# Kernel optimization log

Measured on AMD Instinct MI355X. Metric: run time of the kernel, lower is better.

Reference implementation:

```python
import jax, jax.numpy as jnp
import numpy as np

HIDDEN = 4096
NUM_HEADS = 32
NUM_KV_HEADS = 8
HEAD_DIM = 128
T = 2048
ROPE_THETA = 10000.0


def setup_inputs() -> dict:
    key = jax.random.key(0)
    ks = jax.random.split(key, 10)
    s = 0.02
    return {
        "hidden_states": jax.random.normal(ks[0], (T, HIDDEN), dtype=jnp.float32),
        "positions": jnp.arange(T, dtype=jnp.int32),
        "Wq": jax.random.normal(ks[1], (NUM_HEADS * HEAD_DIM, HIDDEN), dtype=jnp.float32) * s,
        "bq": jax.random.normal(ks[2], (NUM_HEADS * HEAD_DIM,), dtype=jnp.float32) * s,
        "Wk": jax.random.normal(ks[3], (NUM_KV_HEADS * HEAD_DIM, HIDDEN), dtype=jnp.float32) * s,
        "bk": jax.random.normal(ks[4], (NUM_KV_HEADS * HEAD_DIM,), dtype=jnp.float32) * s,
        "Wv": jax.random.normal(ks[5], (NUM_KV_HEADS * HEAD_DIM, HIDDEN), dtype=jnp.float32) * s,
        "bv": jax.random.normal(ks[6], (NUM_KV_HEADS * HEAD_DIM,), dtype=jnp.float32) * s,
        "Wo": jax.random.normal(ks[7], (HIDDEN, HIDDEN), dtype=jnp.float32) * s,
        "bo": jax.random.normal(ks[8], (HIDDEN,), dtype=jnp.float32) * s,
    }


def _rope_cos_sin(positions, head_dim, base):
    # neox-style rotary over the full head_dim
    half = head_dim // 2
    inv_freq = 1.0 / (base ** (jnp.arange(0, half, dtype=jnp.float32) * 2.0 / head_dim))
    angles = positions.astype(jnp.float32)[:, None] * inv_freq[None, :]  # [T, half]
    return jnp.cos(angles), jnp.sin(angles)


def _apply_rope(x, cos, sin):
    # x: [T, H, D]; neox: split halves, rotate
    half = x.shape[-1] // 2
    x1, x2 = x[..., :half], x[..., half:]
    c = cos[:, None, :]
    s = sin[:, None, :]
    return jnp.concatenate([x1 * c - x2 * s, x2 * c + x1 * s], axis=-1)


def reference(hidden_states, positions, Wq, bq, Wk, bk, Wv, bv, Wo, bo):
    q = (hidden_states @ Wq.T + bq).reshape(T, NUM_HEADS, HEAD_DIM)
    k = (hidden_states @ Wk.T + bk).reshape(T, NUM_KV_HEADS, HEAD_DIM)
    v = (hidden_states @ Wv.T + bv).reshape(T, NUM_KV_HEADS, HEAD_DIM)

    cos, sin = _rope_cos_sin(positions, HEAD_DIM, ROPE_THETA)
    q = _apply_rope(q, cos, sin)
    k = _apply_rope(k, cos, sin)

    scale = 1.0 / np.sqrt(HEAD_DIM).astype(np.float32)
    group = NUM_HEADS // NUM_KV_HEADS
    qg = q.reshape(T, NUM_KV_HEADS, group, HEAD_DIM)
    # scores: [g_kv, r, q, k] without materializing repeated KV heads
    scores = jnp.einsum('qgrd,kgd->grqk', qg, k) * scale
    causal = positions[:, None] >= positions[None, :]  # [T, T]
    scores = jnp.where(causal[None, None], scores, jnp.finfo(scores.dtype).min)
    probs = jax.nn.softmax(scores, axis=-1)
    o = jnp.einsum('grqk,kgd->qgrd', probs, v).reshape(T, NUM_HEADS * HEAD_DIM)
    return o @ Wo.T + bo
```

## Files before the change

### kernel.cpp

```cpp
#include <hip/hip_runtime.h>
#include <stdint.h>

typedef unsigned short u16;
typedef __bf16 bf16x8_t __attribute__((ext_vector_type(8)));
typedef float f32x4_t __attribute__((ext_vector_type(4)));

#define T_SEQ 2048
#define HID 4096
#define ROWQKV 6144

__device__ __forceinline__ float bf2f(u16 x){ return __uint_as_float(((uint32_t)x)<<16); }
__device__ __forceinline__ u16 f2bf(float f){
  uint32_t u = __float_as_uint(f);
  return (u16)((u + 0x7fffu + ((u>>16)&1u)) >> 16);
}

__device__ __forceinline__ void gload16(const void* g, void* l){
  __builtin_amdgcn_global_load_lds(
      (const __attribute__((address_space(1))) uint32_t*)g,
      (__attribute__((address_space(3))) uint32_t*)l, 16, 0, 0);
}

__device__ __forceinline__ uint32_t cvtpk(float lo, float hi_){
  uint32_t r;
  asm("v_cvt_pk_bf16_f32 %0, %1, %2" : "=v"(r) : "v"(lo), "v"(hi_));
  return r;
}

__global__ void cvt_kernel(const float* __restrict__ src, u16* __restrict__ dst, int n8){
  int i = blockIdx.x*blockDim.x + threadIdx.x;
  if (i >= n8) return;
  const float4* s = (const float4*)src;
  float4 a = s[2*i], b = s[2*i+1];
  union { u16 u[8]; uint4 v; } o;
  o.u[0]=f2bf(a.x); o.u[1]=f2bf(a.y); o.u[2]=f2bf(a.z); o.u[3]=f2bf(a.w);
  o.u[4]=f2bf(b.x); o.u[5]=f2bf(b.y); o.u[6]=f2bf(b.z); o.u[7]=f2bf(b.w);
  ((uint4*)dst)[i] = o.v;
}

__global__ void setup_kernel(const float* __restrict__ bq, const float* __restrict__ bk,
                             const float* __restrict__ bv, const int* __restrict__ pos,
                             float* __restrict__ bqkv, float* __restrict__ cost,
                             float* __restrict__ sint){
  int i = blockIdx.x*blockDim.x + threadIdx.x;
  if (i < 6144) bqkv[i] = (i<4096) ? bq[i] : ((i<5120) ? bk[i-4096] : bv[i-5120]);
  if (i < T_SEQ*64){
    int t = i >> 6, d = i & 63;
    float inv = powf(10000.0f, -(float)(2*d) / 128.0f);
    float ang = (float)pos[t] * inv;
    cost[i] = cosf(ang);
    sint[i] = sinf(ang);
  }
}

#define GBAR __builtin_amdgcn_s_barrier()
#define LGKM0 do{ asm volatile("s_waitcnt lgkmcnt(0)" ::: "memory"); \
                  __builtin_amdgcn_sched_barrier(0); }while(0)

#define BUF6 28672

#define AREAD6(mh, ck) do{ \
  const u16* ab = &lds[cur + aoff + (mh)*4096]; \
  afr[0] = *(const bf16x8_t*)&ab[0*1024 + (ck)]; \
  afr[1] = *(const bf16x8_t*)&ab[1*1024 + (ck)]; \
  afr[2] = *(const bf16x8_t*)&ab[2*1024 + (ck)]; \
  afr[3] = *(const bf16x8_t*)&ab[3*1024 + (ck)]; }while(0)

#define BREAD6(ck) do{ \
  const u16* bb = &lds[cur + boff]; \
  bfr[0] = *(const bf16x8_t*)&bb[0*1024 + (ck)]; \
  bfr[1] = *(const bf16x8_t*)&bb[1*1024 + (ck)]; \
  bfr[2] = *(const bf16x8_t*)&bb[2*1024 + (ck)]; }while(0)

#define MM12(mh) do{ \
  _Pragma("unroll") \
  for (int mi=0; mi<4; ++mi){ \
    _Pragma("unroll") \
    for (int n=0; n<3; ++n) \
      acc[(mh)*4+mi][n] = __builtin_amdgcn_mfma_f32_16x16x32_bf16(afr[mi], bfr[n], acc[(mh)*4+mi][n],0,0,0); \
  } }while(0)

__global__ __launch_bounds__(512, 2)
void gemm_qkv(const u16* __restrict__ A, const u16* __restrict__ B,
              const float* __restrict__ bias, u16* __restrict__ Cb,
              int K, int N)
{
  __shared__ u16 lds[2*BUF6];
  const int tid = threadIdx.x, lane = tid & 63, w = tid >> 6;
  const int l15 = lane & 15, l4 = lane >> 4;
  const int wm = w >> 2, wn = w & 3;

  const int nwg = gridDim.x * gridDim.y;
  int flat = blockIdx.y * gridDim.x + blockIdx.x;
  flat = (flat & 7) * (nwg >> 3) + (flat >> 3);
  const int bx = flat % gridDim.x, by = flat / gridDim.x;
  const int bm = by * 256, bn = bx * 192;

  const int srow = w*8 + (lane >> 3);
  const int swc  = ((lane & 7) ^ (lane >> 3)) * 8;
  const u16* pA = A + (size_t)(bm + srow)*K + swc;
  const u16* pB = B + (size_t)(bn + srow)*K + swc;
  const size_t j64 = (size_t)64*K;
  const int wu = w*512;

  const int cA0 = ((0 + l4) ^ (l15 & 7)) * 8;
  const int cA1 = ((4 + l4) ^ (l15 & 7)) * 8;
  const int aoff = (wm*128 + l15) * 64;
  const int boff = 16384 + (wn*48 + l15) * 64;

  f32x4_t acc[8][3] = {};
  const int KT = K >> 6;

  gload16(pA + 0*j64, &lds[0     + wu]);
  gload16(pA + 1*j64, &lds[4096  + wu]);
  gload16(pA + 2*j64, &lds[8192  + wu]);
  gload16(pA + 3*j64, &lds[12288 + wu]);
  gload16(pB + 0*j64, &lds[16384 + wu]);
  gload16(pB + 1*j64, &lds[20480 + wu]);
  gload16(pB + 2*j64, &lds[24576 + wu]);
  pA += 64; pB += 64;
  asm volatile("s_waitcnt vmcnt(0)" ::: "memory");
  GBAR;

  for (int t = 0; t < KT; ++t){
    const int cur = (t & 1) * BUF6;
    const int nxt = ((t + 1) & 1) * BUF6;
    const bool st = (t + 1 < KT);
    bf16x8_t afr[4], bfr[3];

    BREAD6(cA0); AREAD6(0, cA0);
    if (st){
      gload16(pA + 0*j64, &lds[nxt + 0     + wu]);
      gload16(pA + 1*j64, &lds[nxt + 4096  + wu]);
      gload16(pA + 2*j64, &lds[nxt + 8192  + wu]);
      gload16(pA + 3*j64, &lds[nxt + 12288 + wu]);
    }
    GBAR; LGKM0;
    __builtin_amdgcn_s_setprio(1); MM12(0); __builtin_amdgcn_s_setprio(0);
    GBAR;

    AREAD6(1, cA0);
    if (st){
      gload16(pB + 0*j64, &lds[nxt + 16384 + wu]);
      gload16(pB + 1*j64, &lds[nxt + 20480 + wu]);
      gload16(pB + 2*j64, &lds[nxt + 24576 + wu]);
      pA += 64; pB += 64;
    }
    GBAR; LGKM0;
    __builtin_amdgcn_s_setprio(1); MM12(1); __builtin_amdgcn_s_setprio(0);
    GBAR;

    BREAD6(cA1); AREAD6(0, cA1);
    GBAR; LGKM0;
    __builtin_amdgcn_s_setprio(1); MM12(0); __builtin_amdgcn_s_setprio(0);
    GBAR;

    AREAD6(1, cA1);
    GBAR; LGKM0;
    __builtin_amdgcn_s_setprio(1); MM12(1); __builtin_amdgcn_s_setprio(0);
    if (st) asm volatile("s_waitcnt vmcnt(0)" ::: "memory");
    GBAR;
  }

  #pragma unroll
  for (int m=0;m<8;m++){
    #pragma unroll
    for (int n=0;n<3;n++){
      #pragma unroll
      for (int j=0;j<4;j++){
        int row = bm + wm*128 + (m>>2)*64 + (m&3)*16 + l4*4 + j;
        int col = bn + wn*48 + n*16 + l15;
        Cb[(size_t)row*N + col] = f2bf(acc[m][n][j] + bias[col]);
      }
    }
  }
}

#define BUFK 24576

#define KMREAD(ck) do{ \
  afr[0] = *(const bf16x8_t*)&lds[cur + aoff + 0*1024 + (ck)]; \
  afr[1] = *(const bf16x8_t*)&lds[cur + aoff + 1*1024 + (ck)]; \
  afr[2] = *(const bf16x8_t*)&lds[cur + aoff + 2*1024 + (ck)]; \
  afr[3] = *(const bf16x8_t*)&lds[cur + aoff + 3*1024 + (ck)]; \
  bfr[0] = *(const bf16x8_t*)&lds[cur + boff + 0*1024 + (ck)]; \
  bfr[1] = *(const bf16x8_t*)&lds[cur + boff + 1*1024 + (ck)]; \
  bfr[2] = *(const bf16x8_t*)&lds[cur + boff + 2*1024 + (ck)]; \
  bfr[3] = *(const bf16x8_t*)&lds[cur + boff + 3*1024 + (ck)]; }while(0)

#define MM16KM do{ \
  _Pragma("unroll") \
  for (int mi=0; mi<4; ++mi){ \
    _Pragma("unroll") \
    for (int n=0; n<4; ++n) \
      acc[mi][n] = __builtin_amdgcn_mfma_f32_16x16x32_bf16(afr[mi], bfr[n], acc[mi][n],0,0,0); \
  } }while(0)

__global__ __launch_bounds__(512, 2)
void gemm_km(const u16* __restrict__ A, const u16* __restrict__ B,
             const float* __restrict__ bias, float* __restrict__ Cf,
             int K, int N)
{
  __shared__ u16 lds[3*BUFK];
  const int tid = threadIdx.x, lane = tid & 63, w = tid >> 6;
  const int l15 = lane & 15, l4 = lane >> 4;
  const int wm = w >> 1, wn = w & 1;

  const int nwg = gridDim.x * gridDim.y;
  int flat = blockIdx.y * gridDim.x + blockIdx.x;
  flat = (flat & 7) * (nwg >> 3) + (flat >> 3);
  const int bx = flat % gridDim.x, by = flat / gridDim.x;
  const int bm = by * 256, bn = bx * 128;

  const int srow = w*8 + (lane >> 3);
  const int swc  = ((lane & 7) ^ (lane >> 3)) * 8;
  const u16* pA = A + (size_t)(bm + srow)*K + swc;
  const u16* pB = B + (size_t)(bn + srow)*K + swc;
  const size_t j64 = (size_t)64*K;
  const int wu = w*512;

  const int cA0 = ((0 + l4) ^ (l15 & 7)) * 8;
  const int cA1 = ((4 + l4) ^ (l15 & 7)) * 8;
  const int aoff = (wm*64 + l15) * 64;
  const int boff = 16384 + (wn*64 + l15) * 64;

  f32x4_t acc[4][4] = {};
  const int KT = K >> 6;

  gload16(pA + 0*j64,      &lds[0*4096 + wu]);
  gload16(pA + 1*j64,      &lds[1*4096 + wu]);
  gload16(pA + 2*j64,      &lds[2*4096 + wu]);
  gload16(pA + 3*j64,      &lds[3*4096 + wu]);
  gload16(pB + 0*j64,      &lds[16384 + 0*4096 + wu]);
  gload16(pB + 1*j64,      &lds[16384 + 1*4096 + wu]);
  gload16(pA + 64 + 0*j64, &lds[BUFK + 0*4096 + wu]);
  gload16(pA + 64 + 1*j64, &lds[BUFK + 1*4096 + wu]);
  gload16(pA + 64 + 2*j64, &lds[BUFK + 2*4096 + wu]);
  gload16(pA + 64 + 3*j64, &lds[BUFK + 3*4096 + wu]);
  gload16(pB + 64 + 0*j64, &lds[BUFK + 16384 + 0*4096 + wu]);
  gload16(pB + 64 + 1*j64, &lds[BUFK + 16384 + 1*4096 + wu]);
  pA += 128; pB += 128;
  asm volatile("s_waitcnt vmcnt(6)" ::: "memory");
  GBAR;

  for (int t = 0; t < KT; ++t){
    const int cur = (t % 3) * BUFK;
    const int sb  = ((t + 2) % 3) * BUFK;
    const bool st = (t + 2 < KT);
    bf16x8_t afr[4], bfr[4];

    KMREAD(cA0);
    if (st){
      gload16(pA + 0*j64, &lds[sb + 0*4096 + wu]);
      gload16(pA + 1*j64, &lds[sb + 1*4096 + wu]);
      gload16(pA + 2*j64, &lds[sb + 2*4096 + wu]);
    }
    GBAR; LGKM0;
    __builtin_amdgcn_s_setprio(1); MM16KM; __builtin_amdgcn_s_setprio(0);
    GBAR;

    KMREAD(cA1);
    if (st){
      gload16(pA + 3*j64, &lds[sb + 3*4096 + wu]);
      gload16(pB + 0*j64, &lds[sb + 16384 + 0*4096 + wu]);
      gload16(pB + 1*j64, &lds[sb + 16384 + 1*4096 + wu]);
      pA += 64; pB += 64;
    }
    GBAR; LGKM0;
    __builtin_amdgcn_s_setprio(1); MM16KM; __builtin_amdgcn_s_setprio(0);
    if (st)              asm volatile("s_waitcnt vmcnt(6)" ::: "memory");
    else if (t + 1 < KT) asm volatile("s_waitcnt vmcnt(0)" ::: "memory");
    GBAR;
  }

  #pragma unroll
  for (int mi=0;mi<4;mi++){
    #pragma unroll
    for (int n=0;n<4;n++){
      #pragma unroll
      for (int j=0;j<4;j++){
        int row = bm + wm*64 + mi*16 + l4*4 + j;
        int col = bn + wn*64 + n*16 + l15;
        Cf[(size_t)row*N + col] = acc[mi][n][j] + bias[col];
      }
    }
  }
}

__global__ void rope_kernel(u16* __restrict__ qkv, const float* __restrict__ cost,
                            const float* __restrict__ sint){
  int i = blockIdx.x*blockDim.x + threadIdx.x;
  int t = i / 2560;
  int r = i % 2560;
  int h = r >> 6, d = r & 63;
  int base = (h < 32) ? h*128 : (4096 + (h-32)*128);
  size_t p1 = (size_t)t*ROWQKV + base + d;
  float x1 = bf2f(qkv[p1]), x2 = bf2f(qkv[p1+64]);
  float c = cost[(t<<6)+d], s = sint[(t<<6)+d];
  qkv[p1]    = f2bf(x1*c - x2*s);
  qkv[p1+64] = f2bf(x2*c + x1*s);
}

#define VOFF 16384
#define POFF 24576

__global__ __launch_bounds__(256, 2)
void attn_kernel(const u16* __restrict__ qkv, u16* __restrict__ attn_o)
{
  __shared__ u16 lds[28672];
  const int tid = threadIdx.x, lane = tid&63, wid = tid>>6;
  const int l15 = lane&15, l4 = lane>>4;
  const int l7 = l15 & 7;
  const int h  = blockIdx.x & 31;
  const int qt = 31 - (blockIdx.x >> 5);
  const int q0 = qt * 64;
  const int kvh = h >> 2;
  const u16* Qg = qkv + h*128;
  const u16* Kg = qkv + 4096 + kvh*128;
  const u16* Vg = qkv + 5120 + kvh*128;
  const float c2 = 0.127543147f;

  bf16x8_t qf[4];
  {
    size_t qrow = (size_t)(q0 + wid*16 + l15);
    #pragma unroll
    for (int kk=0;kk<4;kk++)
      qf[kk] = *(const bf16x8_t*)(Qg + qrow*ROWQKV + kk*32 + l4*8);
  }
  float mrow[4] = {-1e30f,-1e30f,-1e30f,-1e30f};
  float lrow[4] = {0.f,0.f,0.f,0.f};
  f32x4_t oacc[8] = {};

  const u16* ksrc[4];
  int kls[4];
  #pragma unroll
  for (int i=0;i<4;i++){
    const int c = wid*4 + i;
    ksrc[i] = Kg + (size_t)((c&7)*8 + (lane>>3))*ROWQKV
               + (c>>3)*64 + ((lane&7)^(lane>>3))*8;
    kls[i] = c*512;
  }
  const int kvp = tid & 31;
  const int vd0 = (tid >> 5) * 16;
  uint4 rv[4];

  #pragma unroll
  for (int i=0;i<4;i++) gload16(ksrc[i], &lds[kls[i]]);
  #pragma unroll
  for (int i=0;i<4;i++) ksrc[i] += (size_t)64*ROWQKV;
  {
    const u16* va = Vg + (size_t)(2*kvp)*ROWQKV + vd0;
    rv[0] = *(const uint4*)va;            rv[1] = *(const uint4*)(va + 8);
    rv[2] = *(const uint4*)(va + ROWQKV); rv[3] = *(const uint4*)(va + ROWQKV + 8);
  }
  __syncthreads();
  {
    const u16* ra = (const u16*)&rv[0]; const u16* rb = (const u16*)&rv[2];
    #pragma unroll
    for (int e=0;e<8;e++)
      *(uint32_t*)&lds[VOFF + (vd0+e)*64 + ((kvp>>2)^(e&7))*8 + 2*(kvp&3)]
          = (uint32_t)ra[e] | ((uint32_t)rb[e] << 16);
    ra = (const u16*)&rv[1]; rb = (const u16*)&rv[3];
    #pragma unroll
    for (int e=0;e<8;e++)
      *(uint32_t*)&lds[VOFF + (vd0+8+e)*64 + ((kvp>>2)^(e&7))*8 + 2*(kvp&3)]
          = (uint32_t)ra[e] | ((uint32_t)rb[e] << 16);
  }
  __syncthreads();

  for (int kt = 0; kt <= qt; ++kt){
    const int kv0 = kt * 64;
    const int kcur = (kt & 1) * 8192;
    const bool pre = (kt < qt);
    if (pre){
      const int knxt = ((kt+1) & 1) * 8192;
      #pragma unroll
      for (int i=0;i<4;i++) gload16(ksrc[i], &lds[knxt + kls[i]]);
      #pragma unroll
      for (int i=0;i<4;i++) ksrc[i] += (size_t)64*ROWQKV;
      const u16* va = Vg + (size_t)(kv0 + 64 + 2*kvp)*ROWQKV + vd0;
      rv[0] = *(const uint4*)va;            rv[1] = *(const uint4*)(va + 8);
      rv[2] = *(const uint4*)(va + ROWQKV); rv[3] = *(const uint4*)(va + ROWQKV + 8);
    }

    f32x4_t sacc[4] = {};
    __builtin_amdgcn_s_setprio(1);
    #pragma unroll
    for (int n=0;n<4;n++){
      #pragma unroll
      for (int kk=0;kk<4;kk++){
        bf16x8_t kf = *(const bf16x8_t*)&lds[kcur + (kk>>1)*4096
                        + (n*16+l15)*64 + (((kk&1)*4 + l4) ^ l7)*8];
        sacc[n] = __builtin_amdgcn_mfma_f32_16x16x32_bf16(qf[kk], kf, sacc[n], 0,0,0);
      }
    }
    __builtin_amdgcn_s_setprio(0);
    float sv[4][4];
    float pmax[4] = {-1e30f,-1e30f,-1e30f,-1e30f};
    bool diag = (kt == qt);
    #pragma unroll
    for (int n=0;n<4;n++){
      int kvcol = kv0 + n*16 + l15;
      #pragma unroll
      for (int j=0;j<4;j++){
        float s = sacc[n][j];
        int qrow = q0 + wid*16 + l4*4 + j;
        if (diag && kvcol > qrow) s = -1e30f;
        sv[n][j] = s;
        pmax[j] = fmaxf(pmax[j], s);
      }
    }
    #pragma unroll
    for (int off=1; off<16; off<<=1){
      #pragma unroll
      for (int j=0;j<4;j++)
        pmax[j] = fmaxf(pmax[j], __shfl_xor(pmax[j], off, 64));
    }
    float esc[4], rsum[4] = {0.f,0.f,0.f,0.f}, mc[4];
    #pragma unroll
    for (int j=0;j<4;j++){
      float mn = fmaxf(mrow[j], pmax[j]);
      esc[j] = exp2f((mrow[j] - mn) * c2);
      mrow[j] = mn;
      mc[j] = mn * c2;
    }
    #pragma unroll
    for (int n=0;n<4;n++){
      #pragma unroll
      for (int j=0;j<4;j++){
        float p = exp2f(fmaf(sv[n][j], c2, -mc[j]));
        sv[n][j] = p;
        rsum[j] += p;
      }
    }
    #pragma unroll
    for (int off=1; off<16; off<<=1){
      #pragma unroll
      for (int j=0;j<4;j++)
        rsum[j] += __shfl_xor(rsum[j], off, 64);
    }
    #pragma unroll
    for (int j=0;j<4;j++) lrow[j] = lrow[j]*esc[j] + rsum[j];
    #pragma unroll
    for (int n=0;n<8;n++){
      #pragma unroll
      for (int j=0;j<4;j++) oacc[n][j] *= esc[j];
    }
    {
      const int r0 = wid*16 + l4*4;
      #pragma unroll
      for (int n=0;n<4;n++){
        uint32_t p01 = cvtpk(sv[n][0], sv[n][1]);
        uint32_t p23 = cvtpk(sv[n][2], sv[n][3]);
        const int cb = n*2 + (l15>>3);
        lds[POFF + (r0+0)*64 + ((cb ^ ((r0+0)&7))*8) + l7] = (u16)p01;
        lds[POFF + (r0+1)*64 + ((cb ^ ((r0+1)&7))*8) + l7] = (u16)(p01 >> 16);
        lds[POFF + (r0+2)*64 + ((cb ^ ((r0+2)&7))*8) + l7] = (u16)p23;
        lds[POFF + (r0+3)*64 + ((cb ^ ((r0+3)&7))*8) + l7] = (u16)(p23 >> 16);
      }
    }
    __builtin_amdgcn_s_setprio(1);
    #pragma unroll
    for (int kk=0;kk<2;kk++){
      const int blk = ((kk*4 + l4) ^ l7)*8;
      bf16x8_t pf = *(const bf16x8_t*)&lds[POFF + (wid*16 + l15)*64 + blk];
      #pragma unroll
      for (int n=0;n<8;n++){
        bf16x8_t vf = *(const bf16x8_t*)&lds[VOFF + (n*16 + l15)*64 + blk];
        oacc[n] = __builtin_amdgcn_mfma_f32_16x16x32_bf16(pf, vf, oacc[n], 0,0,0);
      }
    }
    __builtin_amdgcn_s_setprio(0);
    __syncthreads();
    if (pre){
      const u16* ra = (const u16*)&rv[0]; const u16* rb = (const u16*)&rv[2];
      #pragma unroll
      for (int e=0;e<8;e++)
        *(uint32_t*)&lds[VOFF + (vd0+e)*64 + ((kvp>>2)^(e&7))*8 + 2*(kvp&3)]
            = (uint32_t)ra[e] | ((uint32_t)rb[e] << 16);
      ra = (const u16*)&rv[1]; rb = (const u16*)&rv[3];
      #pragma unroll
      for (int e=0;e<8;e++)
        *(uint32_t*)&lds[VOFF + (vd0+8+e)*64 + ((kvp>>2)^(e&7))*8 + 2*(kvp&3)]
            = (uint32_t)ra[e] | ((uint32_t)rb[e] << 16);
    }
    __syncthreads();
  }

  #pragma unroll
  for (int n=0;n<8;n++){
    #pragma unroll
    for (int j=0;j<4;j++){
      int qrow = q0 + wid*16 + l4*4 + j;
      int col  = h*128 + n*16 + l15;
      attn_o[(size_t)qrow*HID + col] = f2bf(oacc[n][j] / lrow[j]);
    }
  }
}

extern "C" void kernel_launch(void* const* d_in, const int* in_sizes, int n_in,
                              void* d_out, int out_size, void* d_ws, size_t ws_size,
                              hipStream_t stream)
{
  const float* hs = (const float*)d_in[0];
  const int*  pos = (const int*)d_in[1];
  const float* Wq = (const float*)d_in[2];
  const float* bq = (const float*)d_in[3];
  const float* Wk = (const float*)d_in[4];
  const float* bk = (const float*)d_in[5];
  const float* Wv = (const float*)d_in[6];
  const float* bv = (const float*)d_in[7];
  const float* Wo = (const float*)d_in[8];
  const float* bo = (const float*)d_in[9];
  float* out = (float*)d_out;

  char* ws = (char*)d_ws;
  u16* hs_bf   = (u16*)ws;  ws += (size_t)2048*4096*2;
  u16* Wqkv_bf = (u16*)ws;  ws += (size_t)6144*4096*2;
  u16* Wo_bf   = (u16*)ws;  ws += (size_t)4096*4096*2;
  u16* qkv     = (u16*)ws;  ws += (size_t)2048*6144*2;
  u16* attn_b  = (u16*)ws;  ws += (size_t)2048*4096*2;
  float* bqkv  = (float*)ws; ws += (size_t)6144*4;
  float* cost  = (float*)ws; ws += (size_t)2048*64*4;
  float* sint  = (float*)ws; ws += (size_t)2048*64*4;

  {
    int n8 = 2048*4096/8;
    cvt_kernel<<<(n8+255)/256, 256, 0, stream>>>(hs, hs_bf, n8);
    n8 = 4096*4096/8;
    cvt_kernel<<<(n8+255)/256, 256, 0, stream>>>(Wq, Wqkv_bf, n8);
    n8 = 1024*4096/8;
    cvt_kernel<<<(n8+255)/256, 256, 0, stream>>>(Wk, Wqkv_bf + (size_t)4096*4096, n8);
    cvt_kernel<<<(n8+255)/256, 256, 0, stream>>>(Wv, Wqkv_bf + (size_t)5120*4096, n8);
    n8 = 4096*4096/8;
    cvt_kernel<<<(n8+255)/256, 256, 0, stream>>>(Wo, Wo_bf, n8);
  }
  setup_kernel<<<(T_SEQ*64 + 255)/256, 256, 0, stream>>>(bq, bk, bv, pos, bqkv, cost, sint);

  gemm_qkv<<<dim3(6144/192, 2048/256), 512, 0, stream>>>(hs_bf, Wqkv_bf, bqkv, qkv, 4096, 6144);
  rope_kernel<<<(T_SEQ*40*64)/256, 256, 0, stream>>>(qkv, cost, sint);
  attn_kernel<<<1024, 256, 0, stream>>>(qkv, attn_b);
  gemm_km<<<dim3(4096/128, 2048/256), 512, 0, stream>>>(attn_b, Wo_bf, bo, out, 4096, 4096);
}
```

Baseline: 341.2 us.

## Use 128-row query tiles with 8 waves and double-buffered V in attention

```diff
diff --git a/kernel.cpp b/kernel.cpp
--- a/kernel.cpp
+++ b/kernel.cpp
@@ -302,27 +302,30 @@
 }
 
 #define VOFF 16384
-#define POFF 24576
-
-__global__ __launch_bounds__(256, 2)
+#define POFF 32768
+
+__global__ __launch_bounds__(512, 4)
 void attn_kernel(const u16* __restrict__ qkv, u16* __restrict__ attn_o)
 {
-  __shared__ u16 lds[28672];
+  __shared__ u16 lds[40960];
   const int tid = threadIdx.x, lane = tid&63, wid = tid>>6;
   const int l15 = lane&15, l4 = lane>>4;
   const int l7 = l15 & 7;
-  const int h  = blockIdx.x & 31;
-  const int qt = 31 - (blockIdx.x >> 5);
-  const int q0 = qt * 64;
+  const int b = blockIdx.x;
+  const int h = b & 31;
+  const int c = (b < 256) ? (15 - (b >> 5)) : ((b - 256) >> 5);
+  const int qb = c * 128;
+  const int qwb = qb + wid*16;
   const int kvh = h >> 2;
   const u16* Qg = qkv + h*128;
   const u16* Kg = qkv + 4096 + kvh*128;
   const u16* Vg = qkv + 5120 + kvh*128;
   const float c2 = 0.127543147f;
+  const int nt = 2*c + 2;
 
   bf16x8_t qf[4];
   {
-    size_t qrow = (size_t)(q0 + wid*16 + l15);
+    size_t qrow = (size_t)(qwb + l15);
     #pragma unroll
     for (int kk=0;kk<4;kk++)
       qf[kk] = *(const bf16x8_t*)(Qg + qrow*ROWQKV + kk*32 + l4*8);
@@ -331,157 +334,146 @@
   float lrow[4] = {0.f,0.f,0.f,0.f};
   f32x4_t oacc[8] = {};
 
-  const u16* ksrc[4];
-  int kls[4];
+  const u16* ksrc[2];
+  int kls[2];
   #pragma unroll
-  for (int i=0;i<4;i++){
-    const int c = wid*4 + i;
-    ksrc[i] = Kg + (size_t)((c&7)*8 + (lane>>3))*ROWQKV
-               + (c>>3)*64 + ((lane&7)^(lane>>3))*8;
-    kls[i] = c*512;
+  for (int i=0;i<2;i++){
+    const int cc = wid*2 + i;
+    ksrc[i] = Kg + (size_t)((cc&7)*8 + (lane>>3))*ROWQKV
+               + (cc>>3)*64 + ((lane&7)^(lane>>3))*8;
+    kls[i] = cc*512;
   }
   const int kvp = tid & 31;
-  const int vd0 = (tid >> 5) * 16;
-  uint4 rv[4];
-
-  #pragma unroll
-  for (int i=0;i<4;i++) gload16(ksrc[i], &lds[kls[i]]);
-  #pragma unroll
-  for (int i=0;i<4;i++) ksrc[i] += (size_t)64*ROWQKV;
+  const int vd0 = (tid >> 5) * 8;
+  uint4 rv[2];
+
+  gload16(ksrc[0], &lds[kls[0]]);
+  gload16(ksrc[1], &lds[kls[1]]);
+  ksrc[0] += (size_t)64*ROWQKV; ksrc[1] += (size_t)64*ROWQKV;
   {
     const u16* va = Vg + (size_t)(2*kvp)*ROWQKV + vd0;
-    rv[0] = *(const uint4*)va;            rv[1] = *(const uint4*)(va + 8);
-    rv[2] = *(const uint4*)(va + ROWQKV); rv[3] = *(const uint4*)(va + ROWQKV + 8);
-  }
-  __syncthreads();
-  {
-    const u16* ra = (const u16*)&rv[0]; const u16* rb = (const u16*)&rv[2];
+    rv[0] = *(const uint4*)va;
+    rv[1] = *(const uint4*)(va + ROWQKV);
+    const u16* ra = (const u16*)&rv[0]; const u16* rb = (const u16*)&rv[1];
     #pragma unroll
     for (int e=0;e<8;e++)
-      *(uint32_t*)&lds[VOFF + (vd0+e)*64 + ((kvp>>2)^(e&7))*8 + 2*(kvp&3)]
+      *(uint32_t*)&lds[VOFF + (vd0+e)*64 + ((kvp>>2)^e)*8 + 2*(kvp&3)]
           = (uint32_t)ra[e] | ((uint32_t)rb[e] << 16);
-    ra = (const u16*)&rv[1]; rb = (const u16*)&rv[3];
-    #pragma unroll
-    for (int e=0;e<8;e++)
-      *(uint32_t*)&lds[VOFF + (vd0+8+e)*64 + ((kvp>>2)^(e&7))*8 + 2*(kvp&3)]
-          = (uint32_t)ra[e] | ((uint32_t)rb[e] << 16);
   }
   __syncthreads();
 
-  for (int kt = 0; kt <= qt; ++kt){
+  for (int kt = 0; kt < nt; ++kt){
     const int kv0 = kt * 64;
     const int kcur = (kt & 1) * 8192;
-    const bool pre = (kt < qt);
+    const int vcur = VOFF + (kt & 1) * 8192;
+    const bool pre = (kt + 1 < nt);
     if (pre){
       const int knxt = ((kt+1) & 1) * 8192;
-      #pragma unroll
-      for (int i=0;i<4;i++) gload16(ksrc[i], &lds[knxt + kls[i]]);
-      #pragma unroll
-      for (int i=0;i<4;i++) ksrc[i] += (size_t)64*ROWQKV;
+      gload16(ksrc[0], &lds[knxt + kls[0]]);
+      gload16(ksrc[1], &lds[knxt + kls[1]]);
+      ksrc[0] += (size_t)64*ROWQKV; ksrc[1] += (size_t)64*ROWQKV;
       const u16* va = Vg + (size_t)(kv0 + 64 + 2*kvp)*ROWQKV + vd0;
-      rv[0] = *(const uint4*)va;            rv[1] = *(const uint4*)(va + 8);
-      rv[2] = *(const uint4*)(va + ROWQKV); rv[3] = *(const uint4*)(va + ROWQKV + 8);
-    }
-
-    f32x4_t sacc[4] = {};
-    __builtin_amdgcn_s_setprio(1);
-    #pragma unroll
-    for (int n=0;n<4;n++){
-      #pragma unroll
-      for (int kk=0;kk<4;kk++){
-        bf16x8_t kf = *(const bf16x8_t*)&lds[kcur + (kk>>1)*4096
-                        + (n*16+l15)*64 + (((kk&1)*4 + l4) ^ l7)*8];
-        sacc[n] = __builtin_amdgcn_mfma_f32_16x16x32_bf16(qf[kk], kf, sacc[n], 0,0,0);
-      }
-    }
-    __builtin_amdgcn_s_setprio(0);
-    float sv[4][4];
-    float pmax[4] = {-1e30f,-1e30f,-1e30f,-1e30f};
-    bool diag = (kt == qt);
-    #pragma unroll
-    for (int n=0;n<4;n++){
-      int kvcol = kv0 + n*16 + l15;
+      rv[0] = *(const uint4*)va;
+      rv[1] = *(const uint4*)(va + ROWQKV);
+    }
+
+    if (kv0 <= qwb + 15){
+      f32x4_t sacc[4] = {};
+      __builtin_amdgcn_s_setprio(1);
+      #pragma unroll
+      for (int n=0;n<4;n++){
+        #pragma unroll
+        for (int kk=0;kk<4;kk++){
+          bf16x8_t kf = *(const bf16x8_t*)&lds[kcur + (kk>>1)*4096
+                          + (n*16+l15)*64 + (((kk&1)*4 + l4) ^ l7)*8];
+          sacc[n] = __builtin_amdgcn_mfma_f32_16x16x32_bf16(qf[kk], kf, sacc[n], 0,0,0);
+        }
+      }
+      __builtin_amdgcn_s_setprio(0);
+      float sv[4][4];
+      float pmax[4] = {-1e30f,-1e30f,-1e30f,-1e30f};
+      const bool diag = (kv0 + 63 > qwb);
+      #pragma unroll
+      for (int n=0;n<4;n++){
+        int kvcol = kv0 + n*16 + l15;
+        #pragma unroll
+        for (int j=0;j<4;j++){
+          float s = sacc[n][j];
+          int qrow = qwb + l4*4 + j;
+          if (diag && kvcol > qrow) s = -1e30f;
+          sv[n][j] = s;
+          pmax[j] = fmaxf(pmax[j], s);
+        }
+      }
+      #pragma unroll
+      for (int off=1; off<16; off<<=1){
+        #pragma unroll
+        for (int j=0;j<4;j++)
+          pmax[j] = fmaxf(pmax[j], __shfl_xor(pmax[j], off, 64));
+      }
+      float esc[4], rsum[4] = {0.f,0.f,0.f,0.f}, mc[4];
       #pragma unroll
       for (int j=0;j<4;j++){
-        float s = sacc[n][j];
-        int qrow = q0 + wid*16 + l4*4 + j;
-        if (diag && kvcol > qrow) s = -1e30f;
-        sv[n][j] = s;
-        pmax[j] = fmaxf(pmax[j], s);
-      }
-    }
-    #pragma unroll
-    for (int off=1; off<16; off<<=1){
-      #pragma unroll
-      for (int j=0;j<4;j++)
-        pmax[j] = fmaxf(pmax[j], __shfl_xor(pmax[j], off, 64));
-    }
-    float esc[4], rsum[4] = {0.f,0.f,0.f,0.f}, mc[4];
-    #pragma unroll
-    for (int j=0;j<4;j++){
-      float mn = fmaxf(mrow[j], pmax[j]);
-      esc[j] = exp2f((mrow[j] - mn) * c2);
-      mrow[j] = mn;
-      mc[j] = mn * c2;
-    }
-    #pragma unroll
-    for (int n=0;n<4;n++){
-      #pragma unroll
-      for (int j=0;j<4;j++){
-        float p = exp2f(fmaf(sv[n][j], c2, -mc[j]));
-        sv[n][j] = p;
-        rsum[j] += p;
-      }
-    }
-    #pragma unroll
-    for (int off=1; off<16; off<<=1){
-      #pragma unroll
-      for (int j=0;j<4;j++)
-        rsum[j] += __shfl_xor(rsum[j], off, 64);
-    }
-    #pragma unroll
-    for (int j=0;j<4;j++) lrow[j] = lrow[j]*esc[j] + rsum[j];
-    #pragma unroll
-    for (int n=0;n<8;n++){
-      #pragma unroll
-      for (int j=0;j<4;j++) oacc[n][j] *= esc[j];
-    }
-    {
-      const int r0 = wid*16 + l4*4;
+        float mn = fmaxf(mrow[j], pmax[j]);
+        esc[j] = exp2f((mrow[j] - mn) * c2);
+        mrow[j] = mn;
+        mc[j] = mn * c2;
+      }
       #pragma unroll
       for (int n=0;n<4;n++){
-        uint32_t p01 = cvtpk(sv[n][0], sv[n][1]);
-        uint32_t p23 = cvtpk(sv[n][2], sv[n][3]);
-        const int cb = n*2 + (l15>>3);
-        lds[POFF + (r0+0)*64 + ((cb ^ ((r0+0)&7))*8) + l7] = (u16)p01;
-        lds[POFF + (r0+1)*64 + ((cb ^ ((r0+1)&7))*8) + l7] = (u16)(p01 >> 16);
-        lds[POFF + (r0+2)*64 + ((cb ^ ((r0+2)&7))*8) + l7] = (u16)p23;
-        lds[POFF + (r0+3)*64 + ((cb ^ ((r0+3)&7))*8) + l7] = (u16)(p23 >> 16);
-      }
-    }
-    __builtin_amdgcn_s_setprio(1);
-    #pragma unroll
-    for (int kk=0;kk<2;kk++){
-      const int blk = ((kk*4 + l4) ^ l7)*8;
-      bf16x8_t pf = *(const bf16x8_t*)&lds[POFF + (wid*16 + l15)*64 + blk];
+        #pragma unroll
+        for (int j=0;j<4;j++){
+          float p = exp2f(fmaf(sv[n][j], c2, -mc[j]));
+          sv[n][j] = p;
+          rsum[j] += p;
+        }
+      }
+      #pragma unroll
+      for (int off=1; off<16; off<<=1){
+        #pragma unroll
+        for (int j=0;j<4;j++)
+          rsum[j] += __shfl_xor(rsum[j], off, 64);
+      }
+      #pragma unroll
+      for (int j=0;j<4;j++) lrow[j] = lrow[j]*esc[j] + rsum[j];
       #pragma unroll
       for (int n=0;n<8;n++){
-        bf16x8_t vf = *(const bf16x8_t*)&lds[VOFF + (n*16 + l15)*64 + blk];
-        oacc[n] = __builtin_amdgcn_mfma_f32_16x16x32_bf16(pf, vf, oacc[n], 0,0,0);
-      }
-    }
-    __builtin_amdgcn_s_setprio(0);
-    __syncthreads();
+        #pragma unroll
+        for (int j=0;j<4;j++) oacc[n][j] *= esc[j];
+      }
+      {
+        const int r0 = wid*16 + l4*4;
+        #pragma unroll
+        for (int n=0;n<4;n++){
+          uint32_t p01 = cvtpk(sv[n][0], sv[n][1]);
+          uint32_t p23 = cvtpk(sv[n][2], sv[n][3]);
+          const int cb = n*2 + (l15>>3);
+          lds[POFF + (r0+0)*64 + ((cb ^ ((r0+0)&7))*8) + l7] = (u16)p01;
+          lds[POFF + (r0+1)*64 + ((cb ^ ((r0+1)&7))*8) + l7] = (u16)(p01 >> 16);
+          lds[POFF + (r0+2)*64 + ((cb ^ ((r0+2)&7))*8) + l7] = (u16)p23;
+          lds[POFF + (r0+3)*64 + ((cb ^ ((r0+3)&7))*8) + l7] = (u16)(p23 >> 16);
+        }
+      }
+      __builtin_amdgcn_s_setprio(1);
+      #pragma unroll
+      for (int kk=0;kk<2;kk++){
+        const int blk = ((kk*4 + l4) ^ l7)*8;
+        bf16x8_t pf = *(const bf16x8_t*)&lds[POFF + (wid*16 + l15)*64 + blk];
+        #pragma unroll
+        for (int n=0;n<8;n++){
+          bf16x8_t vf = *(const bf16x8_t*)&lds[vcur + (n*16 + l15)*64 + blk];
+          oacc[n] = __builtin_amdgcn_mfma_f32_16x16x32_bf16(pf, vf, oacc[n], 0,0,0);
+        }
+      }
+      __builtin_amdgcn_s_setprio(0);
+    }
+
     if (pre){
-      const u16* ra = (const u16*)&rv[0]; const u16* rb = (const u16*)&rv[2];
+      const int vnxt = VOFF + ((kt+1) & 1) * 8192;
+      const u16* ra = (const u16*)&rv[0]; const u16* rb = (const u16*)&rv[1];
       #pragma unroll
       for (int e=0;e<8;e++)
-        *(uint32_t*)&lds[VOFF + (vd0+e)*64 + ((kvp>>2)^(e&7))*8 + 2*(kvp&3)]
-            = (uint32_t)ra[e] | ((uint32_t)rb[e] << 16);
-      ra = (const u16*)&rv[1]; rb = (const u16*)&rv[3];
-      #pragma unroll
-      for (int e=0;e<8;e++)
-        *(uint32_t*)&lds[VOFF + (vd0+8+e)*64 + ((kvp>>2)^(e&7))*8 + 2*(kvp&3)]
+        *(uint32_t*)&lds[vnxt + (vd0+e)*64 + ((kvp>>2)^e)*8 + 2*(kvp&3)]
             = (uint32_t)ra[e] | ((uint32_t)rb[e] << 16);
     }
     __syncthreads();
@@ -491,7 +483,7 @@
   for (int n=0;n<8;n++){
     #pragma unroll
     for (int j=0;j<4;j++){
-      int qrow = q0 + wid*16 + l4*4 + j;
+      int qrow = qwb + l4*4 + j;
       int col  = h*128 + n*16 + l15;
       attn_o[(size_t)qrow*HID + col] = f2bf(oacc[n][j] / lrow[j]);
     }
@@ -539,6 +531,6 @@
 
   gemm_qkv<<<dim3(6144/192, 2048/256), 512, 0, stream>>>(hs_bf, Wqkv_bf, bqkv, qkv, 4096, 6144);
   rope_kernel<<<(T_SEQ*40*64)/256, 256, 0, stream>>>(qkv, cost, sint);
-  attn_kernel<<<1024, 256, 0, stream>>>(qkv, attn_b);
+  attn_kernel<<<512, 512, 0, stream>>>(qkv, attn_b);
   gemm_km<<<dim3(4096/128, 2048/256), 512, 0, stream>>>(attn_b, Wo_bf, bo, out, 4096, 4096);
 }
```

Result: slower. 487.5 us (+42.9%).
